# Performance work log

Measured on AMD Instinct MI355X. Metric: run time of the kernel, lower is better.

The kernel has to match this reference:

```python
import jax, jax.numpy as jnp
import numpy as np

N, F_IN, HID, HEADS, NEA, E, G = 50000, 32, 64, 2, 2, 800000, 50
SLOPE = 0.2  # leaky_relu negative_slope


def setup_inputs() -> dict:
    key = jax.random.key(0)
    ks = jax.random.split(key, 24)
    x = jax.random.normal(ks[0], (N, F_IN), jnp.float32)
    src = jax.random.randint(ks[1], (E,), 0, N, jnp.int32)
    off = jax.random.randint(ks[2], (E,), 1, N, jnp.int32)
    dst = ((src + off) % N).astype(jnp.int32)  # guaranteed no self loops
    edge_index = jnp.stack([src, dst])
    edge_attr = jax.random.uniform(ks[3], (E, NEA), jnp.float32, 0.5, 3.0)  # distances (reciprocal taken in fwd)
    batch = (jnp.arange(N) // (N // G)).astype(jnp.int32)
    interface_pos = jnp.arange(0, N, 5, dtype=jnp.int32)  # 200 interface nodes/graph

    def glorot(k, shape, fan_in, fan_out):
        s = jnp.sqrt(6.0 / (fan_in + fan_out))
        return jax.random.uniform(k, shape, jnp.float32, -s, s)

    HC = HEADS * HID
    W0 = glorot(ks[4], (F_IN, HC), F_IN, HC)
    attl0 = glorot(ks[5], (HEADS, HID), HID, HID)
    attr0 = glorot(ks[6], (HEADS, HID), HID, HID)
    W12 = glorot(ks[7], (2, HID, HC), HID, HC)
    attl12 = glorot(ks[8], (2, HEADS, HID), HID, HID)
    attr12 = glorot(ks[9], (2, HEADS, HID), HID, HID)
    eW = glorot(ks[10], (3, NEA, HC), NEA, HC)
    eb = jnp.zeros((3, HC), jnp.float32)
    bconv = jnp.zeros((3, HID), jnp.float32)
    gate_w = glorot(ks[11], (HID, 1), HID, 1)
    gate_b = jnp.zeros((1,), jnp.float32)
    lin1_w = glorot(ks[12], (4 * HID, 2 * HID), 4 * HID, 2 * HID)
    lin1_b = jnp.zeros((2 * HID,), jnp.float32)
    lin2_w = glorot(ks[13], (2 * HID, 1), 2 * HID, 1)
    lin2_b = jnp.zeros((1,), jnp.float32)
    return dict(x=x, edge_index=edge_index, edge_attr=edge_attr, batch=batch,
                interface_pos=interface_pos, graph_num=G,
                W0=W0, attl0=attl0, attr0=attr0, W12=W12, attl12=attl12, attr12=attr12,
                eW=eW, eb=eb, bconv=bconv, gate_w=gate_w, gate_b=gate_b,
                lin1_w=lin1_w, lin1_b=lin1_b, lin2_w=lin2_w, lin2_b=lin2_b)


def segment_softmax(e, seg, n):
    m = jax.ops.segment_max(e, seg, num_segments=n)
    ex = jnp.exp(e - m[seg])
    d = jax.ops.segment_sum(ex, seg, num_segments=n)
    return ex / (d[seg] + 1e-16)


def gate_conv(h, W, att_l, att_r, eW, eb, b, src, dst, ea):
    # GATEConv, concat=False, dropout in eval mode (identity)
    n = h.shape[0]
    H, C = att_l.shape
    xl = (h @ W).reshape(n, H, C)                      # lin_l == lin_r
    al = (xl * att_l).sum(-1)                          # [N,H]
    ar = (xl * att_r).sum(-1)
    e = jax.nn.leaky_relu(al[src] + ar[dst], SLOPE)    # [E+N,H]
    alpha = segment_softmax(e, dst, n)
    ee = (ea @ eW + eb).reshape(-1, H, C)              # edge embeddings
    msg = (xl[src] + ee) * alpha[..., None]
    out = jax.ops.segment_sum(msg, dst, num_segments=n)
    return out.mean(1) + b                             # mean over heads + bias


def reference(x, edge_index, edge_attr, batch, interface_pos, graph_num,
              W0, attl0, attr0, W12, attl12, attr12, eW, eb, bconv,
              gate_w, gate_b, lin1_w, lin1_b, lin2_w, lin2_b):
    n = x.shape[0]
    ar_n = jnp.arange(n, dtype=edge_index.dtype)
    src = jnp.concatenate([edge_index[0], ar_n])       # add self loops
    dst = jnp.concatenate([edge_index[1], ar_n])
    ea = jnp.concatenate([1.0 / edge_attr,
                          jnp.zeros((n, edge_attr.shape[1]), edge_attr.dtype)], 0)

    h = jnp.tanh(gate_conv(x, W0, attl0, attr0, eW[0], eb[0], bconv[0], src, dst, ea))
    xmax = h
    for l in range(2):  # num_layers - 1 structurally distinct weight slices
        h = jnp.tanh(gate_conv(h, W12[l], attl12[l], attr12[l],
                               eW[l + 1], eb[l + 1], bconv[l + 1], src, dst, ea))
        xmax = jnp.maximum(xmax, h)                    # JumpingKnowledge('max')

    xi = xmax[interface_pos]                           # [Ni, hidden]
    bi = batch[interface_pos]
    add = jax.ops.segment_sum(xi, bi, num_segments=graph_num)
    cnt = jax.ops.segment_sum(jnp.ones((xi.shape[0],), xi.dtype), bi, num_segments=graph_num)
    mean = add / jnp.maximum(cnt, 1.0)[:, None]
    gate = (xi @ gate_w + gate_b)[:, 0]                # global self-attention gate
    a = segment_softmax(gate, bi, graph_num)
    attp = jax.ops.segment_sum(a[:, None] * xi, bi, num_segments=graph_num)
    mx = jax.ops.segment_max(xi, bi, num_segments=graph_num)
    pooled = jnp.concatenate([add, mean, attp, mx], -1)  # [G, 4*hidden]
    z = jnp.tanh(pooled @ lin1_w + lin1_b)             # dropout eval = identity
    return z @ lin2_w + lin2_b                         # [G, 1]
```

## Files before the change

kernel.cpp:

```cpp
#include <hip/hip_runtime.h>
#include <hip/hip_bf16.h>
#include <hip/hip_fp16.h>
#include <math.h>

#define N_NODES 50000
#define FIN     32
#define HID     64
#define HC      128
#define NE      800000
#define NET     850000
#define NI      10000
#define NG      50
#define PB      8

typedef _Float16 half8 __attribute__((ext_vector_type(8)));
typedef float float4v __attribute__((ext_vector_type(4)));

__device__ __forceinline__ float lrelu(float x) { return fmaxf(x, 0.2f * x); }

__device__ __forceinline__ unsigned fenc(float f) {
  unsigned u = __float_as_uint(f);
  return (u & 0x80000000u) ? ~u : (u | 0x80000000u);
}
__device__ __forceinline__ float fdec(unsigned u) {
  return (u & 0x80000000u) ? __uint_as_float(u ^ 0x80000000u) : __uint_as_float(~u);
}

__device__ __forceinline__ int rli(int v, int l) {
  return __builtin_amdgcn_readlane(v, l);
}

__global__ void k_histrank(const int* __restrict__ ei, int* __restrict__ deg,
                           int* __restrict__ rank) {
  int e = blockIdx.x * blockDim.x + threadIdx.x;
  if (e >= NET) return;
  int d = (e < NE) ? ei[NE + e] : (e - NE);
  rank[e] = atomicAdd(&deg[d], 1);
}

__global__ void k_base(const int* __restrict__ deg, int* __restrict__ start,
                       int* __restrict__ gcur) {
  __shared__ int buf[256];
  __shared__ int basesh;
  int t = threadIdx.x;
  int i = blockIdx.x * 256 + t;
  int v = (i < N_NODES) ? deg[i] : 0;
  buf[t] = v; __syncthreads();
  for (int off = 1; off < 256; off <<= 1) {
    int a = (t >= off) ? buf[t - off] : 0;
    __syncthreads();
    buf[t] += a;
    __syncthreads();
  }
  if (t == 255) basesh = atomicAdd(gcur, buf[255]);
  __syncthreads();
  if (i < N_NODES) start[i] = basesh + buf[t] - v;
}

__global__ void k_scatter(const int* __restrict__ ei, const float* __restrict__ eattr,
                          const int* __restrict__ start, const int* __restrict__ rank,
                          int2* __restrict__ erec) {
  int e = blockIdx.x * blockDim.x + threadIdx.x;
  if (e >= NET) return;
  int s, d; float ex, ey;
  if (e < NE) {
    s = ei[e]; d = ei[NE + e];
    float2 ea = ((const float2*)eattr)[e];
    ex = 1.0f / ea.x; ey = 1.0f / ea.y;
  } else {
    s = d = e - NE; ex = 0.f; ey = 0.f;
  }
  int pos = start[d] + rank[e];
  __half2 ea2 = __floats2half2_rn(ex, ey);
  erec[pos] = make_int2(s << 8, *(int*)&ea2);
}

template <int F>
__global__ __launch_bounds__(256) void k_linear_mfma(
    const float* __restrict__ h, const float* __restrict__ W,
    const float* __restrict__ attl, const float* __restrict__ attr,
    __half2* __restrict__ xl2h, float* __restrict__ al, float* __restrict__ ar) {
  __shared__ _Float16 hA[16 * F];
  __shared__ _Float16 hC[16 * 128];
  __shared__ float redl[16 * 4], redr[16 * 4];
  const int w = threadIdx.x >> 6, lane = threadIdx.x & 63;
  const int m = lane & 15, q = lane >> 4;
  const int n0 = blockIdx.x * 16;

  for (int i = threadIdx.x; i < 16 * F; i += 256)
    hA[i] = (_Float16)h[(size_t)n0 * F + i];
  __syncthreads();

  half8 a0, a1;
#pragma unroll
  for (int j = 0; j < 8; j++) a0[j] = hA[m * F + q * 8 + j];
  if constexpr (F == 64) {
#pragma unroll
    for (int j = 0; j < 8; j++) a1[j] = hA[m * F + 32 + q * 8 + j];
  }

  const int c0 = w * 32;
  float4v acc[2];
  float pl[4] = {0.f, 0.f, 0.f, 0.f}, pr[4] = {0.f, 0.f, 0.f, 0.f};
#pragma unroll
  for (int t = 0; t < 2; t++) {
    const int colg = c0 + t * 16 + m;
    half8 b0;
#pragma unroll
    for (int j = 0; j < 8; j++) b0[j] = (_Float16)W[(q * 8 + j) * HC + colg];
    float4v z = {0.f, 0.f, 0.f, 0.f};
    acc[t] = __builtin_amdgcn_mfma_f32_16x16x32_f16(a0, b0, z, 0, 0, 0);
    if constexpr (F == 64) {
      half8 b1;
#pragma unroll
      for (int j = 0; j < 8; j++) b1[j] = (_Float16)W[(32 + q * 8 + j) * HC + colg];
      acc[t] = __builtin_amdgcn_mfma_f32_16x16x32_f16(a1, b1, acc[t], 0, 0, 0);
    }
    const float atl = attl[colg], atr = attr[colg];
#pragma unroll
    for (int reg = 0; reg < 4; reg++) {
      float val = acc[t][reg];
      hC[(q * 4 + reg) * 128 + colg] = (_Float16)val;
      pl[reg] += val * atl;
      pr[reg] += val * atr;
    }
  }
#pragma unroll
  for (int off = 1; off < 16; off <<= 1) {
#pragma unroll
    for (int reg = 0; reg < 4; reg++) {
      pl[reg] += __shfl_xor(pl[reg], off, 64);
      pr[reg] += __shfl_xor(pr[reg], off, 64);
    }
  }
  if (m == 0) {
#pragma unroll
    for (int reg = 0; reg < 4; reg++) {
      redl[(q * 4 + reg) * 4 + w] = pl[reg];
      redr[(q * 4 + reg) * 4 + w] = pr[reg];
    }
  }
  __syncthreads();
  if (threadIdx.x < 32) {
    int node = threadIdx.x >> 1, head = threadIdx.x & 1;
    al[(n0 + node) * 2 + head] = redl[node * 4 + head * 2] + redl[node * 4 + head * 2 + 1];
    ar[(n0 + node) * 2 + head] = redr[node * 4 + head * 2] + redr[node * 4 + head * 2 + 1];
  }
  for (int i = threadIdx.x; i < 16 * 64; i += 256) {
    int node = i >> 6, cc = i & 63;
    xl2h[(size_t)(n0 + node) * HID + cc] =
        __halves2half2(hC[node * 128 + cc], hC[node * 128 + 64 + cc]);
  }
}

__global__ void k_aggregate(const __half2* __restrict__ xl2h, const float* __restrict__ alp,
                            const float2* __restrict__ ar2, const int* __restrict__ start,
                            const int* __restrict__ degarr, const int2* __restrict__ erec,
                            const float* __restrict__ eW2, const float* __restrict__ eb1,
                            const float* __restrict__ bconv1, float* __restrict__ hout) {
  const int gid = blockIdx.x * 4 + (threadIdx.x >> 6);
  if (gid >= N_NODES) return;
  const int lane = threadIdx.x & 63;
  const int lane4 = lane << 2;
  const int o0 = start[gid];
  const int deg = degarr[gid];
  const float2 arv = ar2[gid];
  const char* xbase = (const char*)xl2h;
  const char* albase = (const char*)alp;

  const __half2 hz = __floats2half2_rn(0.f, 0.f);
  __half2 accA = hz, accB = hz, accC = hz, accD = hz;
  float ld0 = 0.f, ld1 = 0.f, lex0 = 0.f, ley0 = 0.f, lex1 = 0.f, ley1 = 0.f;
  for (int base = 0; base < deg; base += 64) {
    int j = base + lane;
    int soff = 0, pbits = 0;
    if (j < deg) {
      int2 r = erec[o0 + j];
      soff = r.x;
      float2 eaf = __half22float2(*(__half2*)&r.y);
      float2 alv = *(const float2*)(albase + (soff >> 5));
      float p0 = __expf(lrelu(alv.x + arv.x));
      float p1 = __expf(lrelu(alv.y + arv.y));
      ld0 += p0; ld1 += p1;
      lex0 += p0 * eaf.x; ley0 += p0 * eaf.y;
      lex1 += p1 * eaf.x; ley1 += p1 * eaf.y;
      __half2 ph = __floats2half2_rn(p0, p1);
      pbits = *(int*)&ph;
    }
    int slen = min(64, deg - base);
    int j2 = 0;
    for (; j2 + 8 <= slen; j2 += 8) {
      int so0 = rli(soff, j2),     so1 = rli(soff, j2 + 1);
      int so2 = rli(soff, j2 + 2), so3 = rli(soff, j2 + 3);
      int so4 = rli(soff, j2 + 4), so5 = rli(soff, j2 + 5);
      int so6 = rli(soff, j2 + 6), so7 = rli(soff, j2 + 7);
      __half2 x0 = *(const __half2*)(xbase + so0 + lane4);
      __half2 x1 = *(const __half2*)(xbase + so1 + lane4);
      __half2 x2 = *(const __half2*)(xbase + so2 + lane4);
      __half2 x3 = *(const __half2*)(xbase + so3 + lane4);
      __half2 x4 = *(const __half2*)(xbase + so4 + lane4);
      __half2 x5 = *(const __half2*)(xbase + so5 + lane4);
      __half2 x6 = *(const __half2*)(xbase + so6 + lane4);
      __half2 x7 = *(const __half2*)(xbase + so7 + lane4);
      int pw0 = rli(pbits, j2),     pw1 = rli(pbits, j2 + 1);
      int pw2 = rli(pbits, j2 + 2), pw3 = rli(pbits, j2 + 3);
      int pw4 = rli(pbits, j2 + 4), pw5 = rli(pbits, j2 + 5);
      int pw6 = rli(pbits, j2 + 6), pw7 = rli(pbits, j2 + 7);
      accA = __hfma2(*(__half2*)&pw0, x0, accA);
      accB = __hfma2(*(__half2*)&pw1, x1, accB);
      accC = __hfma2(*(__half2*)&pw2, x2, accC);
      accD = __hfma2(*(__half2*)&pw3, x3, accD);
      accA = __hfma2(*(__half2*)&pw4, x4, accA);
      accB = __hfma2(*(__half2*)&pw5, x5, accB);
      accC = __hfma2(*(__half2*)&pw6, x6, accC);
      accD = __hfma2(*(__half2*)&pw7, x7, accD);
    }
    for (; j2 + 4 <= slen; j2 += 4) {
      int so0 = rli(soff, j2),     so1 = rli(soff, j2 + 1);
      int so2 = rli(soff, j2 + 2), so3 = rli(soff, j2 + 3);
      __half2 x0 = *(const __half2*)(xbase + so0 + lane4);
      __half2 x1 = *(const __half2*)(xbase + so1 + lane4);
      __half2 x2 = *(const __half2*)(xbase + so2 + lane4);
      __half2 x3 = *(const __half2*)(xbase + so3 + lane4);
      int pw0 = rli(pbits, j2),     pw1 = rli(pbits, j2 + 1);
      int pw2 = rli(pbits, j2 + 2), pw3 = rli(pbits, j2 + 3);
      accA = __hfma2(*(__half2*)&pw0, x0, accA);
      accB = __hfma2(*(__half2*)&pw1, x1, accB);
      accC = __hfma2(*(__half2*)&pw2, x2, accC);
      accD = __hfma2(*(__half2*)&pw3, x3, accD);
    }
    for (; j2 < slen; j2++) {
      int so0 = rli(soff, j2);
      __half2 x0 = *(const __half2*)(xbase + so0 + lane4);
      int pw0 = rli(pbits, j2);
      accA = __hfma2(*(__half2*)&pw0, x0, accA);
    }
  }
  float2 fA = __half22float2(accA), fB = __half22float2(accB);
  float2 fC = __half22float2(accC), fD = __half22float2(accD);
  float acc0 = (fA.x + fB.x) + (fC.x + fD.x);
  float acc1 = (fA.y + fB.y) + (fC.y + fD.y);
#pragma unroll
  for (int off = 32; off; off >>= 1) {
    ld0  += __shfl_xor(ld0, off, 64);
    ld1  += __shfl_xor(ld1, off, 64);
    lex0 += __shfl_xor(lex0, off, 64);
    ley0 += __shfl_xor(ley0, off, 64);
    lex1 += __shfl_xor(lex1, off, 64);
    ley1 += __shfl_xor(ley1, off, 64);
  }
  float t0 = acc0 + eW2[lane]      * lex0 + eW2[HC + lane]      * ley0 + eb1[lane]      * ld0;
  float t1 = acc1 + eW2[64 + lane] * lex1 + eW2[HC + 64 + lane] * ley1 + eb1[64 + lane] * ld1;
  float r = 0.5f * (t0 / (ld0 + 1e-16f) + t1 / (ld1 + 1e-16f)) + bconv1[lane];
  hout[(size_t)gid * HID + lane] = tanhf(r);
}

__global__ void k_ranges(const int* __restrict__ ipos, const int* __restrict__ batch,
                         int* __restrict__ gstart) {
  int i = blockIdx.x * blockDim.x + threadIdx.x;
  if (i >= NI) return;
  int bi = batch[ipos[i]];
  int prev = (i > 0) ? batch[ipos[i - 1]] : -1;
  for (int g = prev + 1; g <= bi; g++) gstart[g] = i;
  if (i == NI - 1)
    for (int g = bi + 1; g <= NG; g++) gstart[g] = NI;
}

__global__ void k_pool(const float* __restrict__ h0, const float* __restrict__ h1,
                       const float* __restrict__ h2, const int* __restrict__ ipos,
                       const int* __restrict__ gstart, const float* __restrict__ gate_w,
                       const float* __restrict__ gate_b, float* __restrict__ add,
                       unsigned* __restrict__ mxE, float* __restrict__ cnt,
                       float* __restrict__ attp, float* __restrict__ aden) {
  __shared__ float red[4][3 * HID + 2];
  const int g = blockIdx.x / PB, m = blockIdx.x % PB;
  const int w = threadIdx.x >> 6, lane = threadIdx.x & 63;
  const int s0 = gstart[g], s1 = gstart[g + 1];
  const int len = s1 - s0;
  const int b0 = s0 + (len * m) / PB;
  const int b1 = s0 + (len * (m + 1)) / PB;
  const float gwv = gate_w[lane];
  const float gbv = gate_b[0];

  float padd = 0.f, pmax = -1e30f, pattp = 0.f, paden = 0.f, pcnt = 0.f;
  for (int i = b0 + w; i < b1; i += 4) {
    size_t node = (size_t)ipos[i] * HID + lane;
    float v = fmaxf(fmaxf(h0[node], h1[node]), h2[node]);
    padd += v;
    pmax = fmaxf(pmax, v);
    float gv = v * gwv;
#pragma unroll
    for (int off = 32; off; off >>= 1) gv += __shfl_xor(gv, off, 64);
    float e = __expf(gv + gbv);
    pattp += e * v;
    paden += e;
    pcnt += 1.f;
  }
  red[w][lane] = padd;
  red[w][HID + lane] = pmax;
  red[w][2 * HID + lane] = pattp;
  if (lane == 0) { red[w][3 * HID] = paden; red[w][3 * HID + 1] = pcnt; }
  __syncthreads();
  if (w == 0) {
    float addv  = red[0][lane] + red[1][lane] + red[2][lane] + red[3][lane];
    float maxv  = fmaxf(fmaxf(red[0][HID + lane], red[1][HID + lane]),
                        fmaxf(red[2][HID + lane], red[3][HID + lane]));
    float attpv = red[0][2 * HID + lane] + red[1][2 * HID + lane] +
                  red[2][2 * HID + lane] + red[3][2 * HID + lane];
    atomicAdd(&add[g * HID + lane], addv);
    atomicMax(&mxE[g * HID + lane], fenc(maxv));
    atomicAdd(&attp[g * HID + lane], attpv);
    if (lane == 0) {
      atomicAdd(&aden[g], red[0][3 * HID] + red[1][3 * HID] + red[2][3 * HID] + red[3][3 * HID]);
      atomicAdd(&cnt[g],  red[0][3 * HID + 1] + red[1][3 * HID + 1] +
                          red[2][3 * HID + 1] + red[3][3 * HID + 1]);
    }
  }
}

__global__ void k_final(const float* __restrict__ add, const float* __restrict__ cnt,
                        const float* __restrict__ attp, const float* __restrict__ aden,
                        const unsigned* __restrict__ mxE, const float* __restrict__ lin1_w,
                        const float* __restrict__ lin1_b, const float* __restrict__ lin2_w,
                        const float* __restrict__ lin2_b, float* __restrict__ out) {
  __shared__ float pooled[4 * HID];
  __shared__ float zred[2 * HID];
  int g = blockIdx.x, t = threadIdx.x;
  if (t < HID)            pooled[t] = add[g * HID + t];
  else if (t < 2 * HID)   pooled[t] = add[g * HID + (t - HID)] / fmaxf(cnt[g], 1.f);
  else if (t < 3 * HID)   pooled[t] = attp[g * HID + (t - 2 * HID)] / (aden[g] + 1e-16f);
  else                    pooled[t] = fdec(mxE[g * HID + (t - 3 * HID)]);
  __syncthreads();
  if (t < 2 * HID) {
    float z = lin1_b[t];
    for (int k = 0; k < 4 * HID; k++) z += pooled[k] * lin1_w[k * (2 * HID) + t];
    z = tanhf(z);
    zred[t] = z * lin2_w[t];
  }
  __syncthreads();
  if (t == 0) {
    float s = 0.f;
    for (int k = 0; k < 2 * HID; k++) s += zred[k];
    out[g] = s + lin2_b[0];
  }
}

extern "C" void kernel_launch(void* const* d_in, const int* in_sizes, int n_in,
                              void* d_out, int out_size, void* d_ws, size_t ws_size,
                              hipStream_t stream) {
  const float* x      = (const float*)d_in[0];
  const int*   ei     = (const int*)d_in[1];
  const float* eattr  = (const float*)d_in[2];
  const int*   batch  = (const int*)d_in[3];
  const int*   ipos   = (const int*)d_in[4];
  const float* W0     = (const float*)d_in[6];
  const float* attl0  = (const float*)d_in[7];
  const float* attr0  = (const float*)d_in[8];
  const float* W12    = (const float*)d_in[9];
  const float* attl12 = (const float*)d_in[10];
  const float* attr12 = (const float*)d_in[11];
  const float* eW     = (const float*)d_in[12];
  const float* eb     = (const float*)d_in[13];
  const float* bconv  = (const float*)d_in[14];
  const float* gate_w = (const float*)d_in[15];
  const float* gate_b = (const float*)d_in[16];
  const float* lin1_w = (const float*)d_in[17];
  const float* lin1_b = (const float*)d_in[18];
  const float* lin2_w = (const float*)d_in[19];
  const float* lin2_b = (const float*)d_in[20];
  float* out = (float*)d_out;

  char* ws = (char*)d_ws;
  size_t off = 0;
  auto alloc = [&](size_t elems) {
    void* p = ws + off;
    off += ((elems * 4 + 15) / 16) * 16;
    return p;
  };
  int*      deg    = (int*)alloc(N_NODES);
  int*      gcur   = (int*)alloc(4);
  float*    addp   = (float*)alloc(NG * HID);
  float*    attp   = (float*)alloc(NG * HID);
  unsigned* mxE    = (unsigned*)alloc(NG * HID);
  float*    cnt    = (float*)alloc(64);
  float*    aden   = (float*)alloc(64);
  size_t zbytes = off;
  int*     gstart = (int*)alloc(NG + 4);
  int*     start  = (int*)alloc(N_NODES);
  int*     rank   = (int*)alloc(NET);
  int2*    erec   = (int2*)alloc((size_t)NET * 2);
  __half2* xl2h   = (__half2*)alloc((size_t)N_NODES * HID);
  float*   al     = (float*)alloc((size_t)N_NODES * 2);
  float*   arr    = (float*)alloc((size_t)N_NODES * 2);
  float*   h0     = (float*)alloc((size_t)N_NODES * HID);
  float*   h1     = (float*)alloc((size_t)N_NODES * HID);
  float*   h2     = (float*)alloc((size_t)N_NODES * HID);
  (void)ws_size; (void)in_sizes; (void)n_in; (void)out_size;

  hipMemsetAsync(d_ws, 0, zbytes, stream);
  k_histrank<<<(NET + 255) / 256, 256, 0, stream>>>(ei, deg, rank);
  k_base<<<(N_NODES + 255) / 256, 256, 0, stream>>>(deg, start, gcur);
  k_scatter<<<(NET + 255) / 256, 256, 0, stream>>>(ei, eattr, start, rank, erec);
  k_ranges<<<(NI + 255) / 256, 256, 0, stream>>>(ipos, batch, gstart);

  k_linear_mfma<FIN><<<N_NODES / 16, 256, 0, stream>>>(x, W0, attl0, attr0, xl2h, al, arr);
  k_aggregate<<<N_NODES / 4, 256, 0, stream>>>(xl2h, al, (const float2*)arr,
                                               start, deg, erec, eW, eb, bconv, h0);
  k_linear_mfma<HID><<<N_NODES / 16, 256, 0, stream>>>(h0, W12, attl12, attr12, xl2h, al, arr);
  k_aggregate<<<N_NODES / 4, 256, 0, stream>>>(xl2h, al, (const float2*)arr,
                                               start, deg, erec, eW + 2 * HC, eb + HC,
                                               bconv + HID, h1);
  k_linear_mfma<HID><<<N_NODES / 16, 256, 0, stream>>>(h1, W12 + (size_t)HID * HC,
                                                       attl12 + HC, attr12 + HC, xl2h, al, arr);
  k_aggregate<<<N_NODES / 4, 256, 0, stream>>>(xl2h, al, (const float2*)arr,
                                               start, deg, erec, eW + 4 * HC, eb + 2 * HC,
                                               bconv + 2 * HID, h2);

  k_pool<<<NG * PB, 256, 0, stream>>>(h0, h1, h2, ipos, gstart, gate_w, gate_b,
                                      addp, mxE, cnt, attp, aden);
  k_final<<<NG, 256, 0, stream>>>(addp, cnt, attp, aden, mxE, lin1_w, lin1_b, lin2_w, lin2_b, out);
}
```

Measured before the change: 343.1 us.

## Fuse setup kernels, merge scatter into first linear, store activations in fp16

Folds the interface-range computation into the histogram kernel and the edge scatter into the first-layer linear kernel, which removes two launches. Layer outputs h0/h1/h2 are now stored as fp16 rather than fp32, halving their write and read traffic in the linear and pooling kernels. In exchange, activations lose precision, and the fused scatter runs before the linear work in every block, which adds work to that kernel's critical path.

```diff
diff --git a/kernel.cpp b/kernel.cpp
--- a/kernel.cpp
+++ b/kernel.cpp
@@ -25,17 +25,27 @@
 __device__ __forceinline__ float fdec(unsigned u) {
   return (u & 0x80000000u) ? __uint_as_float(u ^ 0x80000000u) : __uint_as_float(~u);
 }
-
 __device__ __forceinline__ int rli(int v, int l) {
   return __builtin_amdgcn_readlane(v, l);
 }
 
 __global__ void k_histrank(const int* __restrict__ ei, int* __restrict__ deg,
-                           int* __restrict__ rank) {
-  int e = blockIdx.x * blockDim.x + threadIdx.x;
-  if (e >= NET) return;
-  int d = (e < NE) ? ei[NE + e] : (e - NE);
-  rank[e] = atomicAdd(&deg[d], 1);
+                           int* __restrict__ rank, const int* __restrict__ ipos,
+                           const int* __restrict__ batch, int* __restrict__ gstart) {
+  const int gtid = blockIdx.x * blockDim.x + threadIdx.x;
+  const int gstride = gridDim.x * blockDim.x;
+  if (gtid < NET) {
+    int e = gtid;
+    int d = (e < NE) ? ei[NE + e] : (e - NE);
+    rank[e] = atomicAdd(&deg[d], 1);
+  }
+  for (int i = gtid; i < NI; i += gstride) {
+    int bi = batch[ipos[i]];
+    int prev = (i > 0) ? batch[ipos[i - 1]] : -1;
+    for (int g = prev + 1; g <= bi; g++) gstart[g] = i;
+    if (i == NI - 1)
+      for (int g = bi + 1; g <= NG; g++) gstart[g] = NI;
+  }
 }
 
 __global__ void k_base(const int* __restrict__ deg, int* __restrict__ start,
@@ -57,50 +67,35 @@
   if (i < N_NODES) start[i] = basesh + buf[t] - v;
 }
 
-__global__ void k_scatter(const int* __restrict__ ei, const float* __restrict__ eattr,
-                          const int* __restrict__ start, const int* __restrict__ rank,
-                          int2* __restrict__ erec) {
-  int e = blockIdx.x * blockDim.x + threadIdx.x;
-  if (e >= NET) return;
-  int s, d; float ex, ey;
-  if (e < NE) {
-    s = ei[e]; d = ei[NE + e];
-    float2 ea = ((const float2*)eattr)[e];
-    ex = 1.0f / ea.x; ey = 1.0f / ea.y;
-  } else {
-    s = d = e - NE; ex = 0.f; ey = 0.f;
-  }
-  int pos = start[d] + rank[e];
-  __half2 ea2 = __floats2half2_rn(ex, ey);
-  erec[pos] = make_int2(s << 8, *(int*)&ea2);
-}
-
-template <int F>
-__global__ __launch_bounds__(256) void k_linear_mfma(
-    const float* __restrict__ h, const float* __restrict__ W,
+struct ShLin {
+  _Float16 hA[16 * HID];
+  _Float16 hC[16 * HC];
+  float redl[64], redr[64];
+};
+
+template <int F, typename T>
+__device__ __forceinline__ void linear_body(
+    const T* __restrict__ h, const float* __restrict__ W,
     const float* __restrict__ attl, const float* __restrict__ attr,
-    __half2* __restrict__ xl2h, float* __restrict__ al, float* __restrict__ ar) {
-  __shared__ _Float16 hA[16 * F];
-  __shared__ _Float16 hC[16 * 128];
-  __shared__ float redl[16 * 4], redr[16 * 4];
+    __half2* __restrict__ xl2h, float* __restrict__ al, float* __restrict__ ar,
+    ShLin& sh) {
   const int w = threadIdx.x >> 6, lane = threadIdx.x & 63;
   const int m = lane & 15, q = lane >> 4;
   const int n0 = blockIdx.x * 16;
 
   for (int i = threadIdx.x; i < 16 * F; i += 256)
-    hA[i] = (_Float16)h[(size_t)n0 * F + i];
+    sh.hA[i] = (_Float16)h[(size_t)n0 * F + i];
   __syncthreads();
 
   half8 a0, a1;
 #pragma unroll
-  for (int j = 0; j < 8; j++) a0[j] = hA[m * F + q * 8 + j];
+  for (int j = 0; j < 8; j++) a0[j] = sh.hA[m * F + q * 8 + j];
   if constexpr (F == 64) {
 #pragma unroll
-    for (int j = 0; j < 8; j++) a1[j] = hA[m * F + 32 + q * 8 + j];
+    for (int j = 0; j < 8; j++) a1[j] = sh.hA[m * F + 32 + q * 8 + j];
   }
 
   const int c0 = w * 32;
-  float4v acc[2];
   float pl[4] = {0.f, 0.f, 0.f, 0.f}, pr[4] = {0.f, 0.f, 0.f, 0.f};
 #pragma unroll
   for (int t = 0; t < 2; t++) {
@@ -108,19 +103,19 @@
     half8 b0;
 #pragma unroll
     for (int j = 0; j < 8; j++) b0[j] = (_Float16)W[(q * 8 + j) * HC + colg];
-    float4v z = {0.f, 0.f, 0.f, 0.f};
-    acc[t] = __builtin_amdgcn_mfma_f32_16x16x32_f16(a0, b0, z, 0, 0, 0);
+    float4v acc = {0.f, 0.f, 0.f, 0.f};
+    acc = __builtin_amdgcn_mfma_f32_16x16x32_f16(a0, b0, acc, 0, 0, 0);
     if constexpr (F == 64) {
       half8 b1;
 #pragma unroll
       for (int j = 0; j < 8; j++) b1[j] = (_Float16)W[(32 + q * 8 + j) * HC + colg];
-      acc[t] = __builtin_amdgcn_mfma_f32_16x16x32_f16(a1, b1, acc[t], 0, 0, 0);
+      acc = __builtin_amdgcn_mfma_f32_16x16x32_f16(a1, b1, acc, 0, 0, 0);
     }
     const float atl = attl[colg], atr = attr[colg];
 #pragma unroll
     for (int reg = 0; reg < 4; reg++) {
-      float val = acc[t][reg];
-      hC[(q * 4 + reg) * 128 + colg] = (_Float16)val;
+      float val = acc[reg];
+      sh.hC[(q * 4 + reg) * 128 + colg] = (_Float16)val;
       pl[reg] += val * atl;
       pr[reg] += val * atr;
     }
@@ -136,28 +131,61 @@
   if (m == 0) {
 #pragma unroll
     for (int reg = 0; reg < 4; reg++) {
-      redl[(q * 4 + reg) * 4 + w] = pl[reg];
-      redr[(q * 4 + reg) * 4 + w] = pr[reg];
+      sh.redl[(q * 4 + reg) * 4 + w] = pl[reg];
+      sh.redr[(q * 4 + reg) * 4 + w] = pr[reg];
     }
   }
   __syncthreads();
   if (threadIdx.x < 32) {
     int node = threadIdx.x >> 1, head = threadIdx.x & 1;
-    al[(n0 + node) * 2 + head] = redl[node * 4 + head * 2] + redl[node * 4 + head * 2 + 1];
-    ar[(n0 + node) * 2 + head] = redr[node * 4 + head * 2] + redr[node * 4 + head * 2 + 1];
+    al[(n0 + node) * 2 + head] = sh.redl[node * 4 + head * 2] + sh.redl[node * 4 + head * 2 + 1];
+    ar[(n0 + node) * 2 + head] = sh.redr[node * 4 + head * 2] + sh.redr[node * 4 + head * 2 + 1];
   }
   for (int i = threadIdx.x; i < 16 * 64; i += 256) {
     int node = i >> 6, cc = i & 63;
     xl2h[(size_t)(n0 + node) * HID + cc] =
-        __halves2half2(hC[node * 128 + cc], hC[node * 128 + 64 + cc]);
-  }
+        __halves2half2(sh.hC[node * 128 + cc], sh.hC[node * 128 + 64 + cc]);
+  }
+}
+
+__global__ __launch_bounds__(256) void k_linear_h(
+    const _Float16* __restrict__ h, const float* __restrict__ W,
+    const float* __restrict__ attl, const float* __restrict__ attr,
+    __half2* __restrict__ xl2h, float* __restrict__ al, float* __restrict__ ar) {
+  __shared__ ShLin sh;
+  linear_body<HID, _Float16>(h, W, attl, attr, xl2h, al, ar, sh);
+}
+
+__global__ __launch_bounds__(256) void k_scatlin0(
+    const int* __restrict__ ei, const float* __restrict__ eattr,
+    const int* __restrict__ start, const int* __restrict__ rank,
+    int2* __restrict__ erec,
+    const float* __restrict__ x, const float* __restrict__ W,
+    const float* __restrict__ attl, const float* __restrict__ attr,
+    __half2* __restrict__ xl2h, float* __restrict__ al, float* __restrict__ ar) {
+  __shared__ ShLin sh;
+  const int gstride = gridDim.x * blockDim.x;
+  for (int e = blockIdx.x * blockDim.x + threadIdx.x; e < NET; e += gstride) {
+    int s, d; float ex, ey;
+    if (e < NE) {
+      s = ei[e]; d = ei[NE + e];
+      float2 ea = ((const float2*)eattr)[e];
+      ex = 1.0f / ea.x; ey = 1.0f / ea.y;
+    } else {
+      s = d = e - NE; ex = 0.f; ey = 0.f;
+    }
+    int pos = start[d] + rank[e];
+    __half2 ea2 = __floats2half2_rn(ex, ey);
+    erec[pos] = make_int2(s << 8, *(int*)&ea2);
+  }
+  linear_body<FIN, float>(x, W, attl, attr, xl2h, al, ar, sh);
 }
 
 __global__ void k_aggregate(const __half2* __restrict__ xl2h, const float* __restrict__ alp,
                             const float2* __restrict__ ar2, const int* __restrict__ start,
                             const int* __restrict__ degarr, const int2* __restrict__ erec,
                             const float* __restrict__ eW2, const float* __restrict__ eb1,
-                            const float* __restrict__ bconv1, float* __restrict__ hout) {
+                            const float* __restrict__ bconv1, _Float16* __restrict__ hout) {
   const int gid = blockIdx.x * 4 + (threadIdx.x >> 6);
   if (gid >= N_NODES) return;
   const int lane = threadIdx.x & 63;
@@ -252,22 +280,11 @@
   float t0 = acc0 + eW2[lane]      * lex0 + eW2[HC + lane]      * ley0 + eb1[lane]      * ld0;
   float t1 = acc1 + eW2[64 + lane] * lex1 + eW2[HC + 64 + lane] * ley1 + eb1[64 + lane] * ld1;
   float r = 0.5f * (t0 / (ld0 + 1e-16f) + t1 / (ld1 + 1e-16f)) + bconv1[lane];
-  hout[(size_t)gid * HID + lane] = tanhf(r);
-}
-
-__global__ void k_ranges(const int* __restrict__ ipos, const int* __restrict__ batch,
-                         int* __restrict__ gstart) {
-  int i = blockIdx.x * blockDim.x + threadIdx.x;
-  if (i >= NI) return;
-  int bi = batch[ipos[i]];
-  int prev = (i > 0) ? batch[ipos[i - 1]] : -1;
-  for (int g = prev + 1; g <= bi; g++) gstart[g] = i;
-  if (i == NI - 1)
-    for (int g = bi + 1; g <= NG; g++) gstart[g] = NI;
-}
-
-__global__ void k_pool(const float* __restrict__ h0, const float* __restrict__ h1,
-                       const float* __restrict__ h2, const int* __restrict__ ipos,
+  hout[(size_t)gid * HID + lane] = (_Float16)tanhf(r);
+}
+
+__global__ void k_pool(const _Float16* __restrict__ h0, const _Float16* __restrict__ h1,
+                       const _Float16* __restrict__ h2, const int* __restrict__ ipos,
                        const int* __restrict__ gstart, const float* __restrict__ gate_w,
                        const float* __restrict__ gate_b, float* __restrict__ add,
                        unsigned* __restrict__ mxE, float* __restrict__ cnt,
@@ -285,7 +302,7 @@
   float padd = 0.f, pmax = -1e30f, pattp = 0.f, paden = 0.f, pcnt = 0.f;
   for (int i = b0 + w; i < b1; i += 4) {
     size_t node = (size_t)ipos[i] * HID + lane;
-    float v = fmaxf(fmaxf(h0[node], h1[node]), h2[node]);
+    float v = fmaxf(fmaxf((float)h0[node], (float)h1[node]), (float)h2[node]);
     padd += v;
     pmax = fmaxf(pmax, v);
     float gv = v * gwv;
@@ -372,9 +389,9 @@
 
   char* ws = (char*)d_ws;
   size_t off = 0;
-  auto alloc = [&](size_t elems) {
+  auto alloc = [&](size_t words) {
     void* p = ws + off;
-    off += ((elems * 4 + 15) / 16) * 16;
+    off += ((words * 4 + 15) / 16) * 16;
     return p;
   };
   int*      deg    = (int*)alloc(N_NODES);
@@ -385,33 +402,32 @@
   float*    cnt    = (float*)alloc(64);
   float*    aden   = (float*)alloc(64);
   size_t zbytes = off;
-  int*     gstart = (int*)alloc(NG + 4);
-  int*     start  = (int*)alloc(N_NODES);
-  int*     rank   = (int*)alloc(NET);
-  int2*    erec   = (int2*)alloc((size_t)NET * 2);
-  __half2* xl2h   = (__half2*)alloc((size_t)N_NODES * HID);
-  float*   al     = (float*)alloc((size_t)N_NODES * 2);
-  float*   arr    = (float*)alloc((size_t)N_NODES * 2);
-  float*   h0     = (float*)alloc((size_t)N_NODES * HID);
-  float*   h1     = (float*)alloc((size_t)N_NODES * HID);
-  float*   h2     = (float*)alloc((size_t)N_NODES * HID);
+  int*      gstart = (int*)alloc(NG + 4);
+  int*      start  = (int*)alloc(N_NODES);
+  int*      rank   = (int*)alloc(NET);
+  int2*     erec   = (int2*)alloc((size_t)NET * 2);
+  __half2*  xl2h   = (__half2*)alloc((size_t)N_NODES * HID);
+  float*    al     = (float*)alloc((size_t)N_NODES * 2);
+  float*    arr    = (float*)alloc((size_t)N_NODES * 2);
+  _Float16* h0     = (_Float16*)alloc((size_t)N_NODES * HID / 2);
+  _Float16* h1     = (_Float16*)alloc((size_t)N_NODES * HID / 2);
+  _Float16* h2     = (_Float16*)alloc((size_t)N_NODES * HID / 2);
   (void)ws_size; (void)in_sizes; (void)n_in; (void)out_size;
 
   hipMemsetAsync(d_ws, 0, zbytes, stream);
-  k_histrank<<<(NET + 255) / 256, 256, 0, stream>>>(ei, deg, rank);
+  k_histrank<<<(NET + 255) / 256, 256, 0, stream>>>(ei, deg, rank, ipos, batch, gstart);
   k_base<<<(N_NODES + 255) / 256, 256, 0, stream>>>(deg, start, gcur);
-  k_scatter<<<(NET + 255) / 256, 256, 0, stream>>>(ei, eattr, start, rank, erec);
-  k_ranges<<<(NI + 255) / 256, 256, 0, stream>>>(ipos, batch, gstart);
-
-  k_linear_mfma<FIN><<<N_NODES / 16, 256, 0, stream>>>(x, W0, attl0, attr0, xl2h, al, arr);
+
+  k_scatlin0<<<N_NODES / 16, 256, 0, stream>>>(ei, eattr, start, rank, erec,
+                                               x, W0, attl0, attr0, xl2h, al, arr);
   k_aggregate<<<N_NODES / 4, 256, 0, stream>>>(xl2h, al, (const float2*)arr,
                                                start, deg, erec, eW, eb, bconv, h0);
-  k_linear_mfma<HID><<<N_NODES / 16, 256, 0, stream>>>(h0, W12, attl12, attr12, xl2h, al, arr);
+  k_linear_h<<<N_NODES / 16, 256, 0, stream>>>(h0, W12, attl12, attr12, xl2h, al, arr);
   k_aggregate<<<N_NODES / 4, 256, 0, stream>>>(xl2h, al, (const float2*)arr,
                                                start, deg, erec, eW + 2 * HC, eb + HC,
                                                bconv + HID, h1);
-  k_linear_mfma<HID><<<N_NODES / 16, 256, 0, stream>>>(h1, W12 + (size_t)HID * HC,
-                                                       attl12 + HC, attr12 + HC, xl2h, al, arr);
+  k_linear_h<<<N_NODES / 16, 256, 0, stream>>>(h1, W12 + (size_t)HID * HC,
+                                               attl12 + HC, attr12 + HC, xl2h, al, arr);
   k_aggregate<<<N_NODES / 4, 256, 0, stream>>>(xl2h, al, (const float2*)arr,
                                                start, deg, erec, eW + 4 * HC, eb + 2 * HC,
                                                bconv + 2 * HID, h2);
```

New measurement: 344.6 us. Within noise of the previous version (+0.4%).
